# Kernel optimization log

Hardware: AMD Instinct MI355X
Metric: run time of the kernel (lower is better)

The kernel has to match this reference:

```python
import jax, jax.numpy as jnp
import numpy as np

N = 1_600_000          # total points across all polylines
NUM_SEG = 100_000      # number of polylines (segments for scatter_max)
C_IN = 64
C_OUT = 64
NEG_SLOPE = 0.01       # F.leaky_relu default


def setup_inputs() -> dict:
    key = jax.random.key(0)
    k1, k2, k3, k4 = jax.random.split(key, 4)
    features = jax.random.normal(k1, (N, C_IN), dtype=jnp.float32)
    W = jax.random.normal(k2, (C_OUT, C_IN), dtype=jnp.float32) * (1.0 / np.sqrt(C_IN))
    b = jax.random.normal(k3, (C_OUT,), dtype=jnp.float32) * 0.01
    agg_indices = jax.random.randint(k4, (N,), 0, NUM_SEG, dtype=jnp.int32)
    return {"features": features, "W": W, "b": b, "agg_indices": agg_indices}


def reference(features, W, b, agg_indices):
    # fc: Linear(in_channels, out_channels)  -> [N, C_OUT]
    h = features @ W.T + b
    # leaky_relu (default negative_slope=0.01)
    h = jnp.where(h >= 0, h, NEG_SLOPE * h)
    # scatter_max over segments (dim=0): [NUM_SEG, C_OUT]
    agg = jax.ops.segment_max(h, agg_indices, num_segments=NUM_SEG)
    # guard against empty segments (-inf from segment_max); torch_scatter leaves them 0
    agg = jnp.where(jnp.isfinite(agg), agg, 0.0)
    # gather-broadcast and concat -> [N, 2*C_OUT]
    out = jnp.concatenate([h, agg[agg_indices]], axis=-1)
    return out, agg
```

## Files before the change

### kernel.cpp

```cpp
#include <hip/hip_runtime.h>
#include <stdint.h>

#define C 64
#define CAP 64

typedef __attribute__((ext_vector_type(8))) short short8v;
typedef __attribute__((ext_vector_type(4))) float f32x4;

static __device__ __forceinline__ short f2bf(float f) {
    unsigned u = __float_as_uint(f);
    unsigned r = (u + 0x7FFFu + ((u >> 16) & 1u)) >> 16;
    return (short)r;
}

static __device__ __forceinline__ short8v cvt8(f32x4 lo, f32x4 hi) {
    short8v v;
    v[0] = f2bf(lo[0]); v[1] = f2bf(lo[1]); v[2] = f2bf(lo[2]); v[3] = f2bf(lo[3]);
    v[4] = f2bf(hi[0]); v[5] = f2bf(hi[1]); v[6] = f2bf(hi[2]); v[7] = f2bf(hi[3]);
    return v;
}

#define LOADA(t, L)                                                          \
    {                                                                        \
        const float* a0_ = feat + ((size_t)(t) * 32 + r) * C + q * 8;        \
        const float* a1_ = a0_ + 16 * C;                                     \
        L[0] = __builtin_nontemporal_load((const f32x4*)(a0_));              \
        L[1] = __builtin_nontemporal_load((const f32x4*)(a0_ + 4));          \
        L[2] = __builtin_nontemporal_load((const f32x4*)(a0_ + 32));         \
        L[3] = __builtin_nontemporal_load((const f32x4*)(a0_ + 36));         \
        L[4] = __builtin_nontemporal_load((const f32x4*)(a1_));              \
        L[5] = __builtin_nontemporal_load((const f32x4*)(a1_ + 4));         \
        L[6] = __builtin_nontemporal_load((const f32x4*)(a1_ + 32));         \
        L[7] = __builtin_nontemporal_load((const f32x4*)(a1_ + 36));         \
    }

__global__ __launch_bounds__(256) void k_zero_counts(
    unsigned int* __restrict__ bucket, int nseg)
{
    int i = blockIdx.x * blockDim.x + threadIdx.x;
    if (i < nseg) bucket[(size_t)i * CAP] = 0u;
}

__global__ __launch_bounds__(256) void k_gemm_fill(
    const float* __restrict__ feat, const float* __restrict__ W,
    const float* __restrict__ b, const int* __restrict__ idx,
    float* __restrict__ out, unsigned int* __restrict__ bucket, int N)
{
    const int lane = threadIdx.x & 63;
    const int gw   = blockIdx.x * (blockDim.x >> 6) + (threadIdx.x >> 6);
    const int nw   = gridDim.x * (blockDim.x >> 6);
    const int r    = lane & 15;
    const int q    = lane >> 4;

    short8v wf[4][2];
#pragma unroll
    for (int ct = 0; ct < 4; ++ct)
#pragma unroll
        for (int kh = 0; kh < 2; ++kh) {
            const float* src = W + (size_t)(ct * 16 + r) * C + kh * 32 + q * 8;
            wf[ct][kh] = cvt8(*(const f32x4*)src, *(const f32x4*)(src + 4));
        }
    float bias[4];
#pragma unroll
    for (int ct = 0; ct < 4; ++ct) bias[ct] = b[ct * 16 + r];

    const f32x4 zero = {0.f, 0.f, 0.f, 0.f};
    const int nTiles = N >> 5;

    f32x4 cur[8], nxt[8];
    int t = gw;
    if (t < nTiles) LOADA(t, cur);

    for (; t < nTiles; t += nw) {
        const int tn    = t + nw;
        const int rowid = t * 32 + lane;
        const int seg   = (lane < 32) ? idx[rowid] : 0;

        if (tn < nTiles) LOADA(tn, nxt);

        if (lane < 32) {
            unsigned int old = atomicAdd(&bucket[(size_t)seg * CAP], 1u);
            if (old < CAP - 1)
                bucket[(size_t)seg * CAP + 1 + old] = (unsigned int)rowid;
        }

        short8v A0k0 = cvt8(cur[0], cur[1]), A0k1 = cvt8(cur[2], cur[3]);
        short8v A1k0 = cvt8(cur[4], cur[5]), A1k1 = cvt8(cur[6], cur[7]);

        f32x4 d0[4], d1[4];
#pragma unroll
        for (int ct = 0; ct < 4; ++ct) {
            d0[ct] = __builtin_amdgcn_mfma_f32_16x16x32_bf16(A0k0, wf[ct][0], zero, 0, 0, 0);
            d0[ct] = __builtin_amdgcn_mfma_f32_16x16x32_bf16(A0k1, wf[ct][1], d0[ct], 0, 0, 0);
            d1[ct] = __builtin_amdgcn_mfma_f32_16x16x32_bf16(A1k0, wf[ct][0], zero, 0, 0, 0);
            d1[ct] = __builtin_amdgcn_mfma_f32_16x16x32_bf16(A1k1, wf[ct][1], d1[ct], 0, 0, 0);
        }

        const size_t row0 = (size_t)t * 32 + q * 4;
#pragma unroll
        for (int ct = 0; ct < 4; ++ct)
#pragma unroll
            for (int j = 0; j < 4; ++j) {
                float v0 = d0[ct][j] + bias[ct];
                v0 = fmaxf(v0, 0.01f * v0);
                out[(row0 + j) * (2 * C) + ct * 16 + r] = v0;
                float v1 = d1[ct][j] + bias[ct];
                v1 = fmaxf(v1, 0.01f * v1);
                out[(row0 + 16 + j) * (2 * C) + ct * 16 + r] = v1;
            }

#pragma unroll
        for (int i = 0; i < 8; ++i) cur[i] = nxt[i];
    }
}

__global__ __launch_bounds__(256) void k_reduce_scatter(
    float* __restrict__ out, unsigned int* __restrict__ bucket, int nseg)
{
    const int lane = threadIdx.x & 63;
    const int seg  = blockIdx.x * (blockDim.x >> 6) + (threadIdx.x >> 6);
    if (seg >= nseg) return;
    const int cq = lane >> 4;
    const int cc = (lane & 15) * 4;

    unsigned int* brow = bucket + (size_t)seg * CAP;
    const unsigned int v = brow[lane];
    int cnt = __shfl((int)v, 0, 64);
    if (cnt > CAP - 1) cnt = CAP - 1;

    const float ninf = -__builtin_inff();
    f32x4 acc = {ninf, ninf, ninf, ninf};

    const int ng = (cnt + 3) >> 2;
    for (int base = 0; base < ng; base += 4) {
        int nb = ng - base; if (nb > 4) nb = 4;
        f32x4 hv[4];
#pragma unroll
        for (int u = 0; u < 4; ++u) {
            if (u < nb) {
                int sx   = 4 * (base + u) + cq;
                int slot = (sx < cnt) ? (1 + sx) : 1;
                int row  = __shfl((int)v, slot, 64);
                hv[u] = *(const f32x4*)(out + (size_t)row * (2 * C) + cc);
            }
        }
#pragma unroll
        for (int u = 0; u < 4; ++u) {
            if (u < nb) {
                acc[0] = fmaxf(acc[0], hv[u][0]);
                acc[1] = fmaxf(acc[1], hv[u][1]);
                acc[2] = fmaxf(acc[2], hv[u][2]);
                acc[3] = fmaxf(acc[3], hv[u][3]);
            }
        }
    }

#pragma unroll
    for (int j = 0; j < 4; ++j) {
        float o = __shfl_xor(acc[j], 16, 64);
        acc[j] = fmaxf(acc[j], o);
        o = __shfl_xor(acc[j], 32, 64);
        acc[j] = fmaxf(acc[j], o);
    }

    if (cnt == 0) { acc[0] = 0.f; acc[1] = 0.f; acc[2] = 0.f; acc[3] = 0.f; }

    if (lane < 16)
        *(f32x4*)((float*)brow + cc) = acc;

    for (int g = 0; g < ng; ++g) {
        int s    = 4 * g + cq;
        int slot = (s < cnt) ? (1 + s) : 1;
        int row  = __shfl((int)v, slot, 64);
        float* dst = out + (size_t)row * (2 * C) + C + cc;
        __builtin_nontemporal_store(acc, (f32x4*)dst);
    }
}

extern "C" void kernel_launch(void* const* d_in, const int* in_sizes, int n_in,
                              void* d_out, int out_size, void* d_ws, size_t ws_size,
                              hipStream_t stream)
{
    (void)n_in; (void)d_ws; (void)ws_size;
    const float* feat = (const float*)d_in[0];
    const float* W    = (const float*)d_in[1];
    const float* b    = (const float*)d_in[2];
    const int*   idx  = (const int*)d_in[3];
    float* out = (float*)d_out;

    const int N    = in_sizes[0] / C;
    const int nseg = (out_size - N * 2 * C) / C;

    float* aggOut = out + (size_t)N * 2 * C;
    unsigned int* bucket = (unsigned int*)aggOut;

    k_zero_counts<<<(nseg + 255) / 256, 256, 0, stream>>>(bucket, nseg);
    k_gemm_fill<<<2048, 256, 0, stream>>>(feat, W, b, idx, out, bucket, N);
    k_reduce_scatter<<<(nseg + 3) / 4, 256, 0, stream>>>(out, bucket, nseg);
}
```

Baseline: 428.8 us.

## Stage activations as bf16 in workspace and add a separate expand/gather pass

When the workspace is large enough, the GEMM writes the leaky-relu output as bf16 into a scratch buffer instead of fp32 into the output. The segment max then reads the half-size bf16 rows, and a new streaming kernel writes both halves of the output (upcast h plus the gathered agg) sequentially. This replaces scattered fp32 reads and writes with smaller reads and a coalesced write. In exchange it adds an extra kernel and a round trip through the workspace, and it rounds the h half of the output and agg to bf16, which changes accuracy.

Result: slower. 459.7 us (+7.2%).

```diff
diff --git a/kernel.cpp b/kernel.cpp
--- a/kernel.cpp
+++ b/kernel.cpp
@@ -6,6 +6,7 @@
 
 typedef __attribute__((ext_vector_type(8))) short short8v;
 typedef __attribute__((ext_vector_type(4))) float f32x4;
+typedef __attribute__((ext_vector_type(4))) unsigned short u16x4;
 
 static __device__ __forceinline__ short f2bf(float f) {
     unsigned u = __float_as_uint(f);
@@ -41,6 +42,158 @@
     if (i < nseg) bucket[(size_t)i * CAP] = 0u;
 }
 
+__global__ __launch_bounds__(256) void k_gemm_fill_bf16(
+    const float* __restrict__ feat, const float* __restrict__ W,
+    const float* __restrict__ b, const int* __restrict__ idx,
+    unsigned short* __restrict__ hbf, unsigned int* __restrict__ bucket, int N)
+{
+    const int lane = threadIdx.x & 63;
+    const int gw   = blockIdx.x * (blockDim.x >> 6) + (threadIdx.x >> 6);
+    const int nw   = gridDim.x * (blockDim.x >> 6);
+    const int r    = lane & 15;
+    const int q    = lane >> 4;
+
+    short8v wf[4][2];
+#pragma unroll
+    for (int ct = 0; ct < 4; ++ct)
+#pragma unroll
+        for (int kh = 0; kh < 2; ++kh) {
+            const float* src = W + (size_t)(ct * 16 + r) * C + kh * 32 + q * 8;
+            wf[ct][kh] = cvt8(*(const f32x4*)src, *(const f32x4*)(src + 4));
+        }
+    float bias[4];
+#pragma unroll
+    for (int ct = 0; ct < 4; ++ct) bias[ct] = b[ct * 16 + r];
+
+    const f32x4 zero = {0.f, 0.f, 0.f, 0.f};
+    const int nTiles = N >> 5;
+
+    f32x4 cur[8], nxt[8];
+    int t = gw;
+    if (t < nTiles) LOADA(t, cur);
+
+    for (; t < nTiles; t += nw) {
+        const int tn    = t + nw;
+        const int rowid = t * 32 + lane;
+        const int seg   = (lane < 32) ? idx[rowid] : 0;
+
+        if (tn < nTiles) LOADA(tn, nxt);
+
+        if (lane < 32) {
+            unsigned int old = atomicAdd(&bucket[(size_t)seg * CAP], 1u);
+            if (old < CAP - 1)
+                bucket[(size_t)seg * CAP + 1 + old] = (unsigned int)rowid;
+        }
+
+        short8v A0k0 = cvt8(cur[0], cur[1]), A0k1 = cvt8(cur[2], cur[3]);
+        short8v A1k0 = cvt8(cur[4], cur[5]), A1k1 = cvt8(cur[6], cur[7]);
+
+        f32x4 d0[4], d1[4];
+#pragma unroll
+        for (int ct = 0; ct < 4; ++ct) {
+            d0[ct] = __builtin_amdgcn_mfma_f32_16x16x32_bf16(A0k0, wf[ct][0], zero, 0, 0, 0);
+            d0[ct] = __builtin_amdgcn_mfma_f32_16x16x32_bf16(A0k1, wf[ct][1], d0[ct], 0, 0, 0);
+            d1[ct] = __builtin_amdgcn_mfma_f32_16x16x32_bf16(A1k0, wf[ct][0], zero, 0, 0, 0);
+            d1[ct] = __builtin_amdgcn_mfma_f32_16x16x32_bf16(A1k1, wf[ct][1], d1[ct], 0, 0, 0);
+        }
+
+        const size_t row0 = (size_t)t * 32 + q * 4;
+#pragma unroll
+        for (int ct = 0; ct < 4; ++ct)
+#pragma unroll
+            for (int j = 0; j < 4; ++j) {
+                float v0 = d0[ct][j] + bias[ct];
+                v0 = fmaxf(v0, 0.01f * v0);
+                hbf[(row0 + j) * C + ct * 16 + r] = (unsigned short)f2bf(v0);
+                float v1 = d1[ct][j] + bias[ct];
+                v1 = fmaxf(v1, 0.01f * v1);
+                hbf[(row0 + 16 + j) * C + ct * 16 + r] = (unsigned short)f2bf(v1);
+            }
+
+#pragma unroll
+        for (int i = 0; i < 8; ++i) cur[i] = nxt[i];
+    }
+}
+
+__global__ __launch_bounds__(256) void k_reduce_bf16(
+    const unsigned short* __restrict__ hbf,
+    unsigned int* __restrict__ bucket, int nseg)
+{
+    const int lane = threadIdx.x & 63;
+    const int seg  = blockIdx.x * (blockDim.x >> 6) + (threadIdx.x >> 6);
+    if (seg >= nseg) return;
+    const int cq = lane >> 4;
+    const int cl = lane & 15;
+
+    unsigned int* brow = bucket + (size_t)seg * CAP;
+    const unsigned int v = brow[lane];
+    int cnt = __shfl((int)v, 0, 64);
+    if (cnt > CAP - 1) cnt = CAP - 1;
+
+    const float ninf = -__builtin_inff();
+    f32x4 acc = {ninf, ninf, ninf, ninf};
+
+    const int ng = (cnt + 3) >> 2;
+    for (int base = 0; base < ng; base += 4) {
+        int nb = ng - base; if (nb > 4) nb = 4;
+        u16x4 hv[4];
+#pragma unroll
+        for (int u = 0; u < 4; ++u) {
+            if (u < nb) {
+                int sx   = 4 * (base + u) + cq;
+                int slot = (sx < cnt) ? (1 + sx) : 1;
+                int row  = __shfl((int)v, slot, 64);
+                hv[u] = *(const u16x4*)(hbf + (size_t)row * C + cl * 4);
+            }
+        }
+#pragma unroll
+        for (int u = 0; u < 4; ++u) {
+            if (u < nb) {
+#pragma unroll
+                for (int j = 0; j < 4; ++j) {
+                    float f = __uint_as_float((unsigned)hv[u][j] << 16);
+                    acc[j] = fmaxf(acc[j], f);
+                }
+            }
+        }
+    }
+
+#pragma unroll
+    for (int j = 0; j < 4; ++j) {
+        acc[j] = fmaxf(acc[j], __shfl_xor(acc[j], 16, 64));
+        acc[j] = fmaxf(acc[j], __shfl_xor(acc[j], 32, 64));
+    }
+
+    if (cnt == 0) { acc[0] = 0.f; acc[1] = 0.f; acc[2] = 0.f; acc[3] = 0.f; }
+
+    if (lane < 16)
+        *(f32x4*)((float*)brow + cl * 4) = acc;
+}
+
+__global__ __launch_bounds__(256) void k_expand_gather(
+    const unsigned short* __restrict__ hbf, const f32x4* __restrict__ agg,
+    const int* __restrict__ idx, f32x4* __restrict__ out4, long long total)
+{
+    long long i      = (long long)blockIdx.x * blockDim.x + threadIdx.x;
+    long long stride = (long long)gridDim.x * blockDim.x;
+    for (; i < total; i += stride) {
+        int n = (int)(i >> 5);
+        int q = (int)(i & 31);
+        f32x4 vv;
+        if (q < 16) {
+            u16x4 hb = *(const u16x4*)(hbf + (size_t)n * C + q * 4);
+            vv[0] = __uint_as_float((unsigned)hb[0] << 16);
+            vv[1] = __uint_as_float((unsigned)hb[1] << 16);
+            vv[2] = __uint_as_float((unsigned)hb[2] << 16);
+            vv[3] = __uint_as_float((unsigned)hb[3] << 16);
+        } else {
+            int seg = idx[n];
+            vv = agg[(size_t)seg * 16 + (q - 16)];
+        }
+        __builtin_nontemporal_store(vv, &out4[(size_t)n * 32 + q]);
+    }
+}
+
 __global__ __launch_bounds__(256) void k_gemm_fill(
     const float* __restrict__ feat, const float* __restrict__ W,
     const float* __restrict__ b, const int* __restrict__ idx,
@@ -157,10 +310,8 @@
 
 #pragma unroll
     for (int j = 0; j < 4; ++j) {
-        float o = __shfl_xor(acc[j], 16, 64);
-        acc[j] = fmaxf(acc[j], o);
-        o = __shfl_xor(acc[j], 32, 64);
-        acc[j] = fmaxf(acc[j], o);
+        acc[j] = fmaxf(acc[j], __shfl_xor(acc[j], 16, 64));
+        acc[j] = fmaxf(acc[j], __shfl_xor(acc[j], 32, 64));
     }
 
     if (cnt == 0) { acc[0] = 0.f; acc[1] = 0.f; acc[2] = 0.f; acc[3] = 0.f; }
@@ -181,7 +332,7 @@
                               void* d_out, int out_size, void* d_ws, size_t ws_size,
                               hipStream_t stream)
 {
-    (void)n_in; (void)d_ws; (void)ws_size;
+    (void)n_in;
     const float* feat = (const float*)d_in[0];
     const float* W    = (const float*)d_in[1];
     const float* b    = (const float*)d_in[2];
@@ -195,6 +346,17 @@
     unsigned int* bucket = (unsigned int*)aggOut;
 
     k_zero_counts<<<(nseg + 255) / 256, 256, 0, stream>>>(bucket, nseg);
-    k_gemm_fill<<<2048, 256, 0, stream>>>(feat, W, b, idx, out, bucket, N);
-    k_reduce_scatter<<<(nseg + 3) / 4, 256, 0, stream>>>(out, bucket, nseg);
-}
+
+    const size_t need = (size_t)N * C * sizeof(unsigned short);
+    if (ws_size >= need) {
+        unsigned short* hbf = (unsigned short*)d_ws;
+        k_gemm_fill_bf16<<<2048, 256, 0, stream>>>(feat, W, b, idx, hbf, bucket, N);
+        k_reduce_bf16<<<(nseg + 3) / 4, 256, 0, stream>>>(hbf, bucket, nseg);
+        k_expand_gather<<<4096, 256, 0, stream>>>(hbf, (const f32x4*)aggOut,
+                                                  idx, (f32x4*)out,
+                                                  (long long)N * 32);
+    } else {
+        k_gemm_fill<<<2048, 256, 0, stream>>>(feat, W, b, idx, out, bucket, N);
+        k_reduce_scatter<<<(nseg + 3) / 4, 256, 0, stream>>>(out, bucket, nseg);
+    }
+}
```
